# Kernel tuning notes

Measured on AMD Instinct MI355X. Metric: run time of the kernel, lower is better.

The kernel has to match this reference:

```python
import jax, jax.numpy as jnp
import numpy as np

# Model dims (see init_kwargs): embed_dim=64, heads=8, d_k = n_wires = 8
V, D, H, NQ, L, FFN = 32000, 64, 8, 8, 2, 128
B, S = 16, 1024
LAT, H1, H2, NC = 32, 128, 64, 10
INV_SQRT_DK = 1.0 / float(np.sqrt(NQ))
LN_EPS = 1e-5


def _pos_encoding(s, d):
    pos = jnp.arange(s, dtype=jnp.float32)[:, None]
    div = jnp.exp(jnp.arange(0, d, 2, dtype=jnp.float32) * (-np.log(10000.0) / d))
    pe = jnp.zeros((s, d), dtype=jnp.float32)
    pe = pe.at[:, 0::2].set(jnp.sin(pos * div))
    pe = pe.at[:, 1::2].set(jnp.cos(pos * div))
    return pe


def _layernorm(x, g, b):
    mu = jnp.mean(x, axis=-1, keepdims=True)
    var = jnp.mean(jnp.square(x - mu), axis=-1, keepdims=True)
    return (x - mu) * jax.lax.rsqrt(var + LN_EPS) * g + b


def _quantum_heads(x, theta):
    # Analytic simulation of the per-head 8-qubit VQC:
    #   RX(x_i) RX(theta_i) on wire i, CNOT ring (0->1..6->7, 7->0), measure Z.
    # Heisenberg picture: <Z_j> = prod_{i=0..j} cos(x_i+theta_i) for j>=1,
    # <Z_0> = prod_{i=1..7} cos(x_i+theta_i).
    b, s, _ = x.shape
    a = x.reshape(b, s, H, NQ) + theta            # [B,S,H,NQ]
    c = jnp.cos(a)
    cp = jnp.cumprod(c, axis=-1)
    z0 = jnp.prod(c[..., 1:], axis=-1, keepdims=True)
    return jnp.concatenate([z0, cp[..., 1:]], axis=-1)  # [B,S,H,NQ]


def _quantum_attention(x, theta, combine_W):
    qkv = _quantum_heads(x, theta)                 # [B,S,H,dk]
    q = qkv.transpose(0, 2, 1, 3)                  # [B,H,S,dk]
    scores = jnp.einsum('bhqd,bhkd->bhqk', q, q) * INV_SQRT_DK
    p = jax.nn.softmax(scores, axis=-1)
    out = jnp.einsum('bhqk,bhkd->bhqd', p, q)
    out = out.transpose(0, 2, 1, 3).reshape(x.shape[0], x.shape[1], D)
    return out @ combine_W.T                       # no bias (use_bias=False)


def _quantum_ffn(x, theta, W1, b1, W2, b2):
    # FFN QLayer: RX(x_i) then RY(theta_i), no entanglement -> <Z_i> = cos(theta_i)*cos(x_i)
    # GeneralEncoder only reads the first NQ features of each token.
    z = jnp.cos(x[..., :NQ]) * jnp.cos(theta)      # [B,S,NQ]
    h = jax.nn.relu(z @ W1.T + b1)                 # linear1 then ReLU
    return h @ W2.T + b2                           # linear2


def _forward(tokens, emb_table, attn_theta, combine_W, ln1_g, ln1_b, ln2_g, ln2_b,
             ffn_theta, ffn_W1, ffn_b1, ffn_W2, ffn_b2,
             enc_W1, enc_b1, enc_W2, enc_b2, enc_W3, enc_b3,
             dec_W1, dec_b1, dec_W2, dec_b2, dec_W3, dec_b3, cls_W, cls_b):
    x = emb_table[tokens] + _pos_encoding(tokens.shape[1], D)  # embed + positional
    for l in range(L):  # fixed small number of structurally distinct blocks
        a = _quantum_attention(x, attn_theta[l], combine_W[l])
        x = _layernorm(x + a, ln1_g[l], ln1_b[l])
        f = _quantum_ffn(x, ffn_theta[l], ffn_W1[l], ffn_b1[l], ffn_W2[l], ffn_b2[l])
        x = _layernorm(x + f, ln2_g[l], ln2_b[l])
    pooled = jnp.mean(x, axis=1)                   # [B,D]
    # AutoencoderQuantumNet.forward = decode(encode(x)) (quantum_ffn unused there)
    h = jax.nn.relu(pooled @ enc_W1.T + enc_b1)
    h = jax.nn.relu(h @ enc_W2.T + enc_b2)
    lat = h @ enc_W3.T + enc_b3
    h = jax.nn.relu(lat @ dec_W1.T + dec_b1)
    h = jax.nn.relu(h @ dec_W2.T + dec_b2)
    rec = h @ dec_W3.T + dec_b3                    # [B,D]
    return rec @ cls_W.T + cls_b                   # [B,NC]


def setup_inputs() -> dict:
    key = jax.random.key(0)
    ks = list(jax.random.split(key, 32))
    it = iter(ks)
    def nrm(shape, scale=0.05):
        return (jax.random.normal(next(it), shape) * scale).astype(jnp.float32)
    return {
        'tokens': jax.random.randint(next(it), (B, S), 0, V),
        'emb_table': nrm((V, D), 0.02),
        'attn_theta': nrm((L, NQ), 0.1),
        'combine_W': nrm((L, D, D)),
        'ln1_g': jnp.ones((L, D), jnp.float32), 'ln1_b': jnp.zeros((L, D), jnp.float32),
        'ln2_g': jnp.ones((L, D), jnp.float32), 'ln2_b': jnp.zeros((L, D), jnp.float32),
        'ffn_theta': nrm((L, NQ), 0.1),
        'ffn_W1': nrm((L, FFN, NQ)), 'ffn_b1': jnp.zeros((L, FFN), jnp.float32),
        'ffn_W2': nrm((L, D, FFN)), 'ffn_b2': jnp.zeros((L, D), jnp.float32),
        'enc_W1': nrm((H1, D)), 'enc_b1': jnp.zeros((H1,), jnp.float32),
        'enc_W2': nrm((H2, H1)), 'enc_b2': jnp.zeros((H2,), jnp.float32),
        'enc_W3': nrm((LAT, H2)), 'enc_b3': jnp.zeros((LAT,), jnp.float32),
        'dec_W1': nrm((H2, LAT)), 'dec_b1': jnp.zeros((H2,), jnp.float32),
        'dec_W2': nrm((H1, H2)), 'dec_b2': jnp.zeros((H1,), jnp.float32),
        'dec_W3': nrm((D, H1)), 'dec_b3': jnp.zeros((D,), jnp.float32),
        'cls_W': nrm((NC, D)), 'cls_b': jnp.zeros((NC,), jnp.float32),
    }


def reference(tokens, emb_table, attn_theta, combine_W, ln1_g, ln1_b, ln2_g, ln2_b,
              ffn_theta, ffn_W1, ffn_b1, ffn_W2, ffn_b2,
              enc_W1, enc_b1, enc_W2, enc_b2, enc_W3, enc_b3,
              dec_W1, dec_b1, dec_W2, dec_b2, dec_W3, dec_b3, cls_W, cls_b):
    return _forward(tokens, emb_table, attn_theta, combine_W, ln1_g, ln1_b, ln2_g, ln2_b,
                    ffn_theta, ffn_W1, ffn_b1, ffn_W2, ffn_b2,
                    enc_W1, enc_b1, enc_W2, enc_b2, enc_W3, enc_b3,
                    dec_W1, dec_b1, dec_W2, dec_b2, dec_W3, dec_b3, cls_W, cls_b)
```

## Files before the change

kernel.cpp:

```cpp
#include <hip/hip_runtime.h>
#include <math.h>

typedef _Float16 h2 __attribute__((ext_vector_type(2)));
typedef __fp16 hh4 __attribute__((ext_vector_type(4)));
typedef float f4 __attribute__((ext_vector_type(4)));

#define Bsz 16
#define Ssz 1024
#define TOKENS (Bsz * Ssz)
#define Dd 64
#define Hh 8
#define QTTS 520

#if __has_builtin(__builtin_amdgcn_exp2f)
  #define EXPFN(x) __builtin_amdgcn_exp2f(x)
  #define SQRT_PRESCALE 0.7141921f
#else
  #define EXPFN(x) __expf(x)
  #define SQRT_PRESCALE 0.5946036f
#endif

#if __has_builtin(__builtin_amdgcn_mfma_f32_16x16x16_f16)
  #define MFMA16(a, b, c) __builtin_amdgcn_mfma_f32_16x16x16_f16(a, b, c, 0, 0, 0)
#else
  #define MFMA16(a, b, c) __builtin_amdgcn_mfma_f32_16x16x16f16(a, b, c, 0, 0, 0)
#endif

__device__ __forceinline__ h2 pkrtz(float a, float b) {
#if __has_builtin(__builtin_amdgcn_cvt_pkrtz)
  return __builtin_bit_cast(h2, __builtin_amdgcn_cvt_pkrtz(a, b));
#else
  h2 r; r.x = (_Float16)a; r.y = (_Float16)b; return r;
#endif
}
__device__ __forceinline__ unsigned int as_u32(h2 v) {
  return __builtin_bit_cast(unsigned int, v);
}
__device__ __forceinline__ hh4 bc4(uint2 u) {
  return __builtin_bit_cast(hh4, u);
}

__device__ __forceinline__ void qheads_v(const float* xa, const float* th, float* o) {
  float c0 = __cosf(xa[0] + th[0]), c1 = __cosf(xa[1] + th[1]);
  float c2 = __cosf(xa[2] + th[2]), c3 = __cosf(xa[3] + th[3]);
  float c4 = __cosf(xa[4] + th[4]), c5 = __cosf(xa[5] + th[5]);
  float c6 = __cosf(xa[6] + th[6]), c7 = __cosf(xa[7] + th[7]);
  float cp = c0;
  cp *= c1; o[1] = cp; cp *= c2; o[2] = cp; cp *= c3; o[3] = cp;
  cp *= c4; o[4] = cp; cp *= c5; o[5] = cp; cp *= c6; o[6] = cp;
  cp *= c7; o[7] = cp;
  o[0] = c1 * c2 * c3 * c4 * c5 * c6 * c7;
}

template <int EMBED>
__global__ __launch_bounds__(256, 4) void attn_kernel(
    const float* __restrict__ x, float* __restrict__ xw,
    const int* __restrict__ tokens, const float* __restrict__ emb,
    const float* __restrict__ theta,
    float* __restrict__ o_out, float* __restrict__ ps_out) {
  __shared__ unsigned int qrs[Ssz * 4 + 2];
  __shared__ unsigned int qtt[9 * QTTS];
  int blk = blockIdx.x;
  int bh = blk >> 3, split = blk & 7;
  int b = bh >> 3, h = bh & 7;
  int t = threadIdx.x;

  float th[8];
#pragma unroll
  for (int i = 0; i < 8; i++) th[i] = theta[i];

  float frq[4];
  if (EMBED) {
#pragma unroll
    for (int j = 0; j < 4; j++)
      frq[j] = __expf((float)(2 * (h * 4 + j)) * (-0.14391156831f));
  }

  const float* xb = x + (size_t)b * Ssz * Dd + h * 8;

#pragma unroll
  for (int i = 0; i < 4; i += 2) {
    int k0 = t * 4 + i;
    float xa[8], xc[8];
    if (EMBED) {
      int tokA = tokens[b * Ssz + k0];
      int tokB = tokens[b * Ssz + k0 + 1];
      float4 e0 = *(const float4*)&emb[(size_t)tokA * Dd + h * 8];
      float4 e1 = *(const float4*)&emb[(size_t)tokA * Dd + h * 8 + 4];
      float4 f0 = *(const float4*)&emb[(size_t)tokB * Dd + h * 8];
      float4 f1 = *(const float4*)&emb[(size_t)tokB * Dd + h * 8 + 4];
      float sn, cs;
      __sincosf((float)k0 * frq[0], &sn, &cs); xa[0] = e0.x + sn; xa[1] = e0.y + cs;
      __sincosf((float)k0 * frq[1], &sn, &cs); xa[2] = e0.z + sn; xa[3] = e0.w + cs;
      __sincosf((float)k0 * frq[2], &sn, &cs); xa[4] = e1.x + sn; xa[5] = e1.y + cs;
      __sincosf((float)k0 * frq[3], &sn, &cs); xa[6] = e1.z + sn; xa[7] = e1.w + cs;
      __sincosf((float)(k0 + 1) * frq[0], &sn, &cs); xc[0] = f0.x + sn; xc[1] = f0.y + cs;
      __sincosf((float)(k0 + 1) * frq[1], &sn, &cs); xc[2] = f0.z + sn; xc[3] = f0.w + cs;
      __sincosf((float)(k0 + 1) * frq[2], &sn, &cs); xc[4] = f1.x + sn; xc[5] = f1.y + cs;
      __sincosf((float)(k0 + 1) * frq[3], &sn, &cs); xc[6] = f1.z + sn; xc[7] = f1.w + cs;
      if (split == 0) {
        float4 w0, w1;
        w0.x = xa[0]; w0.y = xa[1]; w0.z = xa[2]; w0.w = xa[3];
        w1.x = xa[4]; w1.y = xa[5]; w1.z = xa[6]; w1.w = xa[7];
        *(float4*)&xw[((size_t)b * Ssz + k0) * Dd + h * 8] = w0;
        *(float4*)&xw[((size_t)b * Ssz + k0) * Dd + h * 8 + 4] = w1;
        w0.x = xc[0]; w0.y = xc[1]; w0.z = xc[2]; w0.w = xc[3];
        w1.x = xc[4]; w1.y = xc[5]; w1.z = xc[6]; w1.w = xc[7];
        *(float4*)&xw[((size_t)b * Ssz + k0 + 1) * Dd + h * 8] = w0;
        *(float4*)&xw[((size_t)b * Ssz + k0 + 1) * Dd + h * 8 + 4] = w1;
      }
    } else {
      float4 v0 = *(const float4*)(xb + (size_t)k0 * Dd);
      float4 v1 = *(const float4*)(xb + (size_t)k0 * Dd + 4);
      float4 v2 = *(const float4*)(xb + (size_t)(k0 + 1) * Dd);
      float4 v3 = *(const float4*)(xb + (size_t)(k0 + 1) * Dd + 4);
      xa[0] = v0.x; xa[1] = v0.y; xa[2] = v0.z; xa[3] = v0.w;
      xa[4] = v1.x; xa[5] = v1.y; xa[6] = v1.z; xa[7] = v1.w;
      xc[0] = v2.x; xc[1] = v2.y; xc[2] = v2.z; xc[3] = v2.w;
      xc[4] = v3.x; xc[5] = v3.y; xc[6] = v3.z; xc[7] = v3.w;
    }
    float oa[8], ob[8];
    qheads_v(xa, th, oa);
    qheads_v(xc, th, ob);
    uint4 wa, wb;
    wa.x = as_u32(pkrtz(oa[0] * SQRT_PRESCALE, oa[1] * SQRT_PRESCALE));
    wa.y = as_u32(pkrtz(oa[2] * SQRT_PRESCALE, oa[3] * SQRT_PRESCALE));
    wa.z = as_u32(pkrtz(oa[4] * SQRT_PRESCALE, oa[5] * SQRT_PRESCALE));
    wa.w = as_u32(pkrtz(oa[6] * SQRT_PRESCALE, oa[7] * SQRT_PRESCALE));
    wb.x = as_u32(pkrtz(ob[0] * SQRT_PRESCALE, ob[1] * SQRT_PRESCALE));
    wb.y = as_u32(pkrtz(ob[2] * SQRT_PRESCALE, ob[3] * SQRT_PRESCALE));
    wb.z = as_u32(pkrtz(ob[4] * SQRT_PRESCALE, ob[5] * SQRT_PRESCALE));
    wb.w = as_u32(pkrtz(ob[6] * SQRT_PRESCALE, ob[7] * SQRT_PRESCALE));
    *(uint4*)&qrs[k0 * 4] = wa;
    *(uint4*)&qrs[(k0 + 1) * 4] = wb;
#pragma unroll
    for (int d = 0; d < 8; d++)
      qtt[d * QTTS + (k0 >> 1)] = as_u32(pkrtz(oa[d], ob[d]));
  }
  for (int j = 8 * QTTS + t; j < 9 * QTTS; j += 256) qtt[j] = 0x3C003C00u;
  if (t == 0) { qrs[Ssz * 4] = 0; qrs[Ssz * 4 + 1] = 0; }
  __syncthreads();

  int l = t & 63, w = t >> 6;
  int g = l >> 4, rr = l & 15;
  int rt0 = split * 8 + w * 2;
  int rowA = rt0 * 16 + rr;
  int rowB = rowA + 16;
  uint2 z2; z2.x = 0; z2.y = 0;
  uint2 buA = (g < 2) ? *(const uint2*)&qrs[rowA * 4 + 2 * g] : z2;
  uint2 buB = (g < 2) ? *(const uint2*)&qrs[rowB * 4 + 2 * g] : z2;
  hh4 BrA = bc4(buA), BrB = bc4(buB);
  int aoff  = (g < 2) ? (rr * 4 + 2 * g) : (Ssz * 4);
  int astep = (g < 2) ? 64 : 0;
  int qrow  = (rr >= 8) ? 8 : rr;
  int qoff  = qrow * QTTS + 2 * g;
  f4 zf = {0.f, 0.f, 0.f, 0.f};
  f4 accA0 = zf, accB0 = zf, accA1 = zf, accB1 = zf;

#pragma unroll 4
  for (int kt = 0; kt < 64; kt += 2) {
    uint2 au0 = *(const uint2*)&qrs[aoff + kt * astep];
    uint2 au1 = *(const uint2*)&qrs[aoff + (kt + 1) * astep];
    uint2 qt0 = *(const uint2*)&qtt[qoff + kt * 8];
    uint2 qt1 = *(const uint2*)&qtt[qoff + (kt + 1) * 8];
    {
      hh4 Ak = bc4(au0);
      f4 sA = MFMA16(Ak, BrA, zf);
      f4 sB = MFMA16(Ak, BrB, zf);
      float pA0 = EXPFN(sA.x), pA1 = EXPFN(sA.y), pA2 = EXPFN(sA.z), pA3 = EXPFN(sA.w);
      float pB0 = EXPFN(sB.x), pB1 = EXPFN(sB.y), pB2 = EXPFN(sB.z), pB3 = EXPFN(sB.w);
      uint2 pbA, pbB;
      pbA.x = as_u32(pkrtz(pA0, pA1)); pbA.y = as_u32(pkrtz(pA2, pA3));
      pbB.x = as_u32(pkrtz(pB0, pB1)); pbB.y = as_u32(pkrtz(pB2, pB3));
      hh4 Aq = bc4(qt0);
      accA0 = MFMA16(Aq, bc4(pbA), accA0);
      accB0 = MFMA16(Aq, bc4(pbB), accB0);
    }
    {
      hh4 Ak = bc4(au1);
      f4 sA = MFMA16(Ak, BrA, zf);
      f4 sB = MFMA16(Ak, BrB, zf);
      float pA0 = EXPFN(sA.x), pA1 = EXPFN(sA.y), pA2 = EXPFN(sA.z), pA3 = EXPFN(sA.w);
      float pB0 = EXPFN(sB.x), pB1 = EXPFN(sB.y), pB2 = EXPFN(sB.z), pB3 = EXPFN(sB.w);
      uint2 pbA, pbB;
      pbA.x = as_u32(pkrtz(pA0, pA1)); pbA.y = as_u32(pkrtz(pA2, pA3));
      pbB.x = as_u32(pkrtz(pB0, pB1)); pbB.y = as_u32(pkrtz(pB2, pB3));
      hh4 Aq = bc4(qt1);
      accA1 = MFMA16(Aq, bc4(pbA), accA1);
      accB1 = MFMA16(Aq, bc4(pbB), accB1);
    }
  }
  f4 accA = accA0 + accA1;
  f4 accB = accB0 + accB1;

  size_t tokA = (size_t)b * Ssz + rowA;
  size_t tokB = (size_t)b * Ssz + rowB;
  if (g < 2) {
    *(f4*)&o_out[tokA * 64 + h * 8 + 4 * g] = accA;
    *(f4*)&o_out[tokB * 64 + h * 8 + 4 * g] = accB;
  } else if (g == 2) {
    ps_out[tokA * 8 + h] = accA.x;
    ps_out[tokB * 8 + h] = accB.x;
  }
}

__global__ __launch_bounds__(64) void tail_kernel(
    float* __restrict__ x, const float* __restrict__ o_out,
    const float* __restrict__ ps_out, const float* __restrict__ Wc,
    const float* __restrict__ g1, const float* __restrict__ bb1,
    const float* __restrict__ g2, const float* __restrict__ bb2,
    const float* __restrict__ fth,
    const float* __restrict__ W1, const float* __restrict__ fb1,
    const float* __restrict__ W2, const float* __restrict__ fb2,
    float* __restrict__ partial, int do_partial) {
  __shared__ float xbuf[16][68];
  int l = threadIdx.x & 63;
  int g = l >> 4, c = l & 15;
  int tok0 = blockIdx.x * 16;
  f4 zf = {0.f, 0.f, 0.f, 0.f};

  {
    hh4 Bf[4][4];
#pragma unroll
    for (int dc = 0; dc < 4; dc++)
#pragma unroll
      for (int kc = 0; kc < 4; kc++) {
        float4 wv = *(const float4*)&Wc[(size_t)(dc * 16 + c) * 64 + kc * 16 + 4 * g];
        uint2 u; u.x = as_u32(pkrtz(wv.x, wv.y)); u.y = as_u32(pkrtz(wv.z, wv.w));
        Bf[kc][dc] = bc4(u);
      }
    int tka = tok0 + c;
    hh4 Af[4];
#pragma unroll
    for (int kc = 0; kc < 4; kc++) {
      float4 o4 = *(const float4*)&o_out[(size_t)tka * 64 + kc * 16 + 4 * g];
      float inv = 1.0f / ps_out[(size_t)tka * 8 + kc * 2 + (g >> 1)];
      uint2 u;
      u.x = as_u32(pkrtz(o4.x * inv, o4.y * inv));
      u.y = as_u32(pkrtz(o4.z * inv, o4.w * inv));
      Af[kc] = bc4(u);
    }
    float yy[4][4];
#pragma unroll
    for (int dc = 0; dc < 4; dc++) {
      f4 acc = zf;
#pragma unroll
      for (int kc = 0; kc < 4; kc++) acc = MFMA16(Af[kc], Bf[kc][dc], acc);
      yy[dc][0] = acc.x; yy[dc][1] = acc.y; yy[dc][2] = acc.z; yy[dc][3] = acc.w;
    }
    float g1v[4], b1v[4];
#pragma unroll
    for (int dc = 0; dc < 4; dc++) { g1v[dc] = g1[dc * 16 + c]; b1v[dc] = bb1[dc * 16 + c]; }
#pragma unroll
    for (int r = 0; r < 4; r++) {
      int tok = tok0 + 4 * g + r;
      float rv0 = x[(size_t)tok * 64 + c]      + yy[0][r];
      float rv1 = x[(size_t)tok * 64 + 16 + c] + yy[1][r];
      float rv2 = x[(size_t)tok * 64 + 32 + c] + yy[2][r];
      float rv3 = x[(size_t)tok * 64 + 48 + c] + yy[3][r];
      float s = (rv0 + rv1) + (rv2 + rv3);
      s += __shfl_xor(s, 1, 64); s += __shfl_xor(s, 2, 64);
      s += __shfl_xor(s, 4, 64); s += __shfl_xor(s, 8, 64);
      float mu = s * (1.f / 64.f);
      float t0 = rv0 - mu, t1 = rv1 - mu, t2 = rv2 - mu, t3 = rv3 - mu;
      float q = (t0 * t0 + t1 * t1) + (t2 * t2 + t3 * t3);
      q += __shfl_xor(q, 1, 64); q += __shfl_xor(q, 2, 64);
      q += __shfl_xor(q, 4, 64); q += __shfl_xor(q, 8, 64);
      float inv = rsqrtf(q * (1.f / 64.f) + 1e-5f);
      int tk = 4 * g + r;
      xbuf[tk][c]      = t0 * inv * g1v[0] + b1v[0];
      xbuf[tk][16 + c] = t1 * inv * g1v[1] + b1v[1];
      xbuf[tk][32 + c] = t2 * inv * g1v[2] + b1v[2];
      xbuf[tk][48 + c] = t3 * inv * g1v[3] + b1v[3];
    }
  }

  float4 x4[4];
#pragma unroll
  for (int dc = 0; dc < 4; dc++)
    x4[dc] = *(const float4*)&xbuf[c][dc * 16 + 4 * g];

  uint2 uz; uz.x = 0; uz.y = 0;
  if (g < 2) {
    float4 thv = *(const float4*)&fth[4 * g];
    float z0 = __cosf(x4[0].x) * __cosf(thv.x);
    float z1 = __cosf(x4[0].y) * __cosf(thv.y);
    float z2 = __cosf(x4[0].z) * __cosf(thv.z);
    float z3 = __cosf(x4[0].w) * __cosf(thv.w);
    uz.x = as_u32(pkrtz(z0, z1)); uz.y = as_u32(pkrtz(z2, z3));
  }
  hh4 Bz = bc4(uz);

  hh4 Bh[8];
#pragma unroll
  for (int jc = 0; jc < 8; jc++) {
    uint2 uw; uw.x = 0; uw.y = 0;
    if (g < 2) {
      float4 wv = *(const float4*)&W1[(size_t)(jc * 16 + c) * 8 + 4 * g];
      uw.x = as_u32(pkrtz(wv.x, wv.y)); uw.y = as_u32(pkrtz(wv.z, wv.w));
    }
    f4 d1 = MFMA16(bc4(uw), Bz, zf);
    float4 b1v = *(const float4*)&fb1[jc * 16 + 4 * g];
    float h0 = fmaxf(d1.x + b1v.x, 0.f);
    float h1 = fmaxf(d1.y + b1v.y, 0.f);
    float h2 = fmaxf(d1.z + b1v.z, 0.f);
    float h3 = fmaxf(d1.w + b1v.w, 0.f);
    uint2 uh;
    uh.x = as_u32(pkrtz(h0, h1)); uh.y = as_u32(pkrtz(h2, h3));
    Bh[jc] = bc4(uh);
  }

  float ff[4][4];
#pragma unroll
  for (int dc = 0; dc < 4; dc++) {
    f4 acc = zf;
#pragma unroll
    for (int kc = 0; kc < 8; kc++) {
      float4 wv = *(const float4*)&W2[(size_t)(dc * 16 + c) * 128 + kc * 16 + 4 * g];
      uint2 uw;
      uw.x = as_u32(pkrtz(wv.x, wv.y)); uw.y = as_u32(pkrtz(wv.z, wv.w));
      acc = MFMA16(bc4(uw), Bh[kc], acc);
    }
    ff[dc][0] = acc.x; ff[dc][1] = acc.y; ff[dc][2] = acc.z; ff[dc][3] = acc.w;
  }

  float r2[4][4];
  float s = 0.f;
#pragma unroll
  for (int dc = 0; dc < 4; dc++) {
    float4 b2v = *(const float4*)&fb2[dc * 16 + 4 * g];
    r2[dc][0] = x4[dc].x + ff[dc][0] + b2v.x;
    r2[dc][1] = x4[dc].y + ff[dc][1] + b2v.y;
    r2[dc][2] = x4[dc].z + ff[dc][2] + b2v.z;
    r2[dc][3] = x4[dc].w + ff[dc][3] + b2v.w;
    s += (r2[dc][0] + r2[dc][1]) + (r2[dc][2] + r2[dc][3]);
  }
  s += __shfl_xor(s, 16, 64); s += __shfl_xor(s, 32, 64);
  float mu = s * (1.f / 64.f);
  float q = 0.f;
#pragma unroll
  for (int dc = 0; dc < 4; dc++) {
#pragma unroll
    for (int r = 0; r < 4; r++) { r2[dc][r] -= mu; q += r2[dc][r] * r2[dc][r]; }
  }
  q += __shfl_xor(q, 16, 64); q += __shfl_xor(q, 32, 64);
  float inv = rsqrtf(q * (1.f / 64.f) + 1e-5f);

  float xo[4][4];
#pragma unroll
  for (int dc = 0; dc < 4; dc++) {
    float4 gv = *(const float4*)&g2[dc * 16 + 4 * g];
    float4 bv = *(const float4*)&bb2[dc * 16 + 4 * g];
    xo[dc][0] = r2[dc][0] * inv * gv.x + bv.x;
    xo[dc][1] = r2[dc][1] * inv * gv.y + bv.y;
    xo[dc][2] = r2[dc][2] * inv * gv.z + bv.z;
    xo[dc][3] = r2[dc][3] * inv * gv.w + bv.w;
    float4 o4;
    o4.x = xo[dc][0]; o4.y = xo[dc][1]; o4.z = xo[dc][2]; o4.w = xo[dc][3];
    *(float4*)&x[(size_t)(tok0 + c) * 64 + dc * 16 + 4 * g] = o4;
  }

  if (do_partial) {
#pragma unroll
    for (int dc = 0; dc < 4; dc++)
#pragma unroll
      for (int r = 0; r < 4; r++) {
        float p = xo[dc][r];
        p += __shfl_xor(p, 1, 64); p += __shfl_xor(p, 2, 64);
        p += __shfl_xor(p, 4, 64); p += __shfl_xor(p, 8, 64);
        xo[dc][r] = p;
      }
    if (c == 0) {
#pragma unroll
      for (int dc = 0; dc < 4; dc++) {
        float4 o4;
        o4.x = xo[dc][0]; o4.y = xo[dc][1]; o4.z = xo[dc][2]; o4.w = xo[dc][3];
        *(float4*)&partial[(size_t)blockIdx.x * 64 + dc * 16 + 4 * g] = o4;
      }
    }
  }
}

__global__ __launch_bounds__(128) void head_kernel(
    const float* __restrict__ partial,
    const float* eW1, const float* eb1, const float* eW2, const float* eb2,
    const float* eW3, const float* eb3, const float* dW1, const float* db1v,
    const float* dW2, const float* db2v, const float* dW3, const float* db3v,
    const float* cW, const float* cb, float* __restrict__ out) {
  __shared__ float bufP[64];
  __shared__ float bufA[128];
  __shared__ float bufB[128];
  int b = blockIdx.x, t = threadIdx.x;
  if (t < 64) {
    float s = 0.f;
    for (int c = 0; c < 64; ++c) s += partial[(size_t)(b * 64 + c) * 64 + t];
    bufP[t] = s * (1.f / 1024.f);
  }
  __syncthreads();
  {
    float v = eb1[t];
    for (int d = 0; d < 64; d++) v = fmaf(bufP[d], eW1[t * 64 + d], v);
    bufA[t] = fmaxf(v, 0.f);
  }
  __syncthreads();
  if (t < 64) {
    float v = eb2[t];
    for (int j = 0; j < 128; j++) v = fmaf(bufA[j], eW2[t * 128 + j], v);
    bufB[t] = fmaxf(v, 0.f);
  }
  __syncthreads();
  if (t < 32) {
    float v = eb3[t];
    for (int d = 0; d < 64; d++) v = fmaf(bufB[d], eW3[t * 64 + d], v);
    bufA[t] = v;
  }
  __syncthreads();
  if (t < 64) {
    float v = db1v[t];
    for (int k = 0; k < 32; k++) v = fmaf(bufA[k], dW1[t * 32 + k], v);
    bufB[t] = fmaxf(v, 0.f);
  }
  __syncthreads();
  {
    float v = db2v[t];
    for (int k = 0; k < 64; k++) v = fmaf(bufB[k], dW2[t * 64 + k], v);
    bufA[t] = fmaxf(v, 0.f);
  }
  __syncthreads();
  if (t < 64) {
    float v = db3v[t];
    for (int j = 0; j < 128; j++) v = fmaf(bufA[j], dW3[t * 128 + j], v);
    bufB[t] = v;
  }
  __syncthreads();
  if (t < 10) {
    float v = cb[t];
    for (int d = 0; d < 64; d++) v = fmaf(bufB[d], cW[t * 64 + d], v);
    out[b * 10 + t] = v;
  }
}

extern "C" void kernel_launch(void* const* d_in, const int* in_sizes, int n_in,
                              void* d_out, int out_size, void* d_ws, size_t ws_size,
                              hipStream_t stream) {
  const int*   tokens     = (const int*)d_in[0];
  const float* emb        = (const float*)d_in[1];
  const float* attn_theta = (const float*)d_in[2];
  const float* combine_W  = (const float*)d_in[3];
  const float* ln1_g      = (const float*)d_in[4];
  const float* ln1_b      = (const float*)d_in[5];
  const float* ln2_g      = (const float*)d_in[6];
  const float* ln2_b      = (const float*)d_in[7];
  const float* ffn_theta  = (const float*)d_in[8];
  const float* ffn_W1     = (const float*)d_in[9];
  const float* ffn_b1     = (const float*)d_in[10];
  const float* ffn_W2     = (const float*)d_in[11];
  const float* ffn_b2     = (const float*)d_in[12];
  const float* enc_W1 = (const float*)d_in[13]; const float* enc_b1 = (const float*)d_in[14];
  const float* enc_W2 = (const float*)d_in[15]; const float* enc_b2 = (const float*)d_in[16];
  const float* enc_W3 = (const float*)d_in[17]; const float* enc_b3 = (const float*)d_in[18];
  const float* dec_W1 = (const float*)d_in[19]; const float* dec_b1 = (const float*)d_in[20];
  const float* dec_W2 = (const float*)d_in[21]; const float* dec_b2 = (const float*)d_in[22];
  const float* dec_W3 = (const float*)d_in[23]; const float* dec_b3 = (const float*)d_in[24];
  const float* cls_W  = (const float*)d_in[25]; const float* cls_b  = (const float*)d_in[26];

  float* x       = (float*)d_ws;
  float* o_out   = x + (size_t)TOKENS * 64;
  float* ps_out  = o_out + (size_t)TOKENS * 64;
  float* partial = ps_out + (size_t)TOKENS * 8;
  float* out     = (float*)d_out;

  attn_kernel<1><<<128 * 8, 256, 0, stream>>>(x, x, tokens, emb,
                                              attn_theta, o_out, ps_out);
  tail_kernel<<<TOKENS / 16, 64, 0, stream>>>(
      x, o_out, ps_out, combine_W,
      ln1_g, ln1_b, ln2_g, ln2_b,
      ffn_theta, ffn_W1, ffn_b1, ffn_W2, ffn_b2, partial, 0);
  attn_kernel<0><<<128 * 8, 256, 0, stream>>>(x, x, tokens, emb,
                                              attn_theta + 8, o_out, ps_out);
  tail_kernel<<<TOKENS / 16, 64, 0, stream>>>(
      x, o_out, ps_out, combine_W + 4096,
      ln1_g + 64, ln1_b + 64, ln2_g + 64, ln2_b + 64,
      ffn_theta + 8, ffn_W1 + 1024, ffn_b1 + 128,
      ffn_W2 + 8192, ffn_b2 + 64, partial, 1);
  head_kernel<<<16, 128, 0, stream>>>(partial, enc_W1, enc_b1, enc_W2, enc_b2,
                                      enc_W3, enc_b3, dec_W1, dec_b1, dec_W2,
                                      dec_b2, dec_W3, dec_b3, cls_W, cls_b, out);
}
```

Measured before the change: 87.42 us.

## Process four query row tiles per wave to reuse key/value LDS loads

```diff
diff --git a/kernel.cpp b/kernel.cpp
--- a/kernel.cpp
+++ b/kernel.cpp
@@ -53,7 +53,7 @@
 }
 
 template <int EMBED>
-__global__ __launch_bounds__(256, 4) void attn_kernel(
+__global__ __launch_bounds__(256, 2) void attn_kernel(
     const float* __restrict__ x, float* __restrict__ xw,
     const int* __restrict__ tokens, const float* __restrict__ emb,
     const float* __restrict__ theta,
@@ -61,7 +61,7 @@
   __shared__ unsigned int qrs[Ssz * 4 + 2];
   __shared__ unsigned int qtt[9 * QTTS];
   int blk = blockIdx.x;
-  int bh = blk >> 3, split = blk & 7;
+  int bh = blk >> 2, split = blk & 3;
   int b = bh >> 3, h = bh & 7;
   int t = threadIdx.x;
 
@@ -143,64 +143,56 @@
 
   int l = t & 63, w = t >> 6;
   int g = l >> 4, rr = l & 15;
-  int rt0 = split * 8 + w * 2;
-  int rowA = rt0 * 16 + rr;
-  int rowB = rowA + 16;
+  int rt0 = split * 16 + w * 4;
+  int row0 = rt0 * 16 + rr;
   uint2 z2; z2.x = 0; z2.y = 0;
-  uint2 buA = (g < 2) ? *(const uint2*)&qrs[rowA * 4 + 2 * g] : z2;
-  uint2 buB = (g < 2) ? *(const uint2*)&qrs[rowB * 4 + 2 * g] : z2;
-  hh4 BrA = bc4(buA), BrB = bc4(buB);
+  hh4 Br[4];
+#pragma unroll
+  for (int j = 0; j < 4; j++) {
+    uint2 bu = (g < 2) ? *(const uint2*)&qrs[(row0 + 16 * j) * 4 + 2 * g] : z2;
+    Br[j] = bc4(bu);
+  }
   int aoff  = (g < 2) ? (rr * 4 + 2 * g) : (Ssz * 4);
   int astep = (g < 2) ? 64 : 0;
   int qrow  = (rr >= 8) ? 8 : rr;
   int qoff  = qrow * QTTS + 2 * g;
   f4 zf = {0.f, 0.f, 0.f, 0.f};
-  f4 accA0 = zf, accB0 = zf, accA1 = zf, accB1 = zf;
-
-#pragma unroll 4
-  for (int kt = 0; kt < 64; kt += 2) {
-    uint2 au0 = *(const uint2*)&qrs[aoff + kt * astep];
-    uint2 au1 = *(const uint2*)&qrs[aoff + (kt + 1) * astep];
-    uint2 qt0 = *(const uint2*)&qtt[qoff + kt * 8];
-    uint2 qt1 = *(const uint2*)&qtt[qoff + (kt + 1) * 8];
-    {
-      hh4 Ak = bc4(au0);
-      f4 sA = MFMA16(Ak, BrA, zf);
-      f4 sB = MFMA16(Ak, BrB, zf);
-      float pA0 = EXPFN(sA.x), pA1 = EXPFN(sA.y), pA2 = EXPFN(sA.z), pA3 = EXPFN(sA.w);
-      float pB0 = EXPFN(sB.x), pB1 = EXPFN(sB.y), pB2 = EXPFN(sB.z), pB3 = EXPFN(sB.w);
-      uint2 pbA, pbB;
-      pbA.x = as_u32(pkrtz(pA0, pA1)); pbA.y = as_u32(pkrtz(pA2, pA3));
-      pbB.x = as_u32(pkrtz(pB0, pB1)); pbB.y = as_u32(pkrtz(pB2, pB3));
-      hh4 Aq = bc4(qt0);
-      accA0 = MFMA16(Aq, bc4(pbA), accA0);
-      accB0 = MFMA16(Aq, bc4(pbB), accB0);
-    }
-    {
-      hh4 Ak = bc4(au1);
-      f4 sA = MFMA16(Ak, BrA, zf);
-      f4 sB = MFMA16(Ak, BrB, zf);
-      float pA0 = EXPFN(sA.x), pA1 = EXPFN(sA.y), pA2 = EXPFN(sA.z), pA3 = EXPFN(sA.w);
-      float pB0 = EXPFN(sB.x), pB1 = EXPFN(sB.y), pB2 = EXPFN(sB.z), pB3 = EXPFN(sB.w);
-      uint2 pbA, pbB;
-      pbA.x = as_u32(pkrtz(pA0, pA1)); pbA.y = as_u32(pkrtz(pA2, pA3));
-      pbB.x = as_u32(pkrtz(pB0, pB1)); pbB.y = as_u32(pkrtz(pB2, pB3));
-      hh4 Aq = bc4(qt1);
-      accA1 = MFMA16(Aq, bc4(pbA), accA1);
-      accB1 = MFMA16(Aq, bc4(pbB), accB1);
-    }
-  }
-  f4 accA = accA0 + accA1;
-  f4 accB = accB0 + accB1;
-
-  size_t tokA = (size_t)b * Ssz + rowA;
-  size_t tokB = (size_t)b * Ssz + rowB;
-  if (g < 2) {
-    *(f4*)&o_out[tokA * 64 + h * 8 + 4 * g] = accA;
-    *(f4*)&o_out[tokB * 64 + h * 8 + 4 * g] = accB;
-  } else if (g == 2) {
-    ps_out[tokA * 8 + h] = accA.x;
-    ps_out[tokB * 8 + h] = accB.x;
+  f4 acc0 = zf, acc1 = zf, acc2 = zf, acc3 = zf;
+
+#pragma unroll 2
+  for (int kt = 0; kt < 64; ++kt) {
+    uint2 au = *(const uint2*)&qrs[aoff + kt * astep];
+    uint2 qt = *(const uint2*)&qtt[qoff + kt * 8];
+    hh4 Ak = bc4(au);
+    hh4 Aq = bc4(qt);
+    f4 s0 = MFMA16(Ak, Br[0], zf);
+    f4 s1 = MFMA16(Ak, Br[1], zf);
+    f4 s2 = MFMA16(Ak, Br[2], zf);
+    f4 s3 = MFMA16(Ak, Br[3], zf);
+    uint2 pb0, pb1, pb2, pb3;
+    pb0.x = as_u32(pkrtz(EXPFN(s0.x), EXPFN(s0.y)));
+    pb0.y = as_u32(pkrtz(EXPFN(s0.z), EXPFN(s0.w)));
+    pb1.x = as_u32(pkrtz(EXPFN(s1.x), EXPFN(s1.y)));
+    pb1.y = as_u32(pkrtz(EXPFN(s1.z), EXPFN(s1.w)));
+    pb2.x = as_u32(pkrtz(EXPFN(s2.x), EXPFN(s2.y)));
+    pb2.y = as_u32(pkrtz(EXPFN(s2.z), EXPFN(s2.w)));
+    pb3.x = as_u32(pkrtz(EXPFN(s3.x), EXPFN(s3.y)));
+    pb3.y = as_u32(pkrtz(EXPFN(s3.z), EXPFN(s3.w)));
+    acc0 = MFMA16(Aq, bc4(pb0), acc0);
+    acc1 = MFMA16(Aq, bc4(pb1), acc1);
+    acc2 = MFMA16(Aq, bc4(pb2), acc2);
+    acc3 = MFMA16(Aq, bc4(pb3), acc3);
+  }
+
+#pragma unroll
+  for (int j = 0; j < 4; j++) {
+    f4 acc = (j == 0) ? acc0 : (j == 1) ? acc1 : (j == 2) ? acc2 : acc3;
+    size_t tok = (size_t)b * Ssz + row0 + 16 * j;
+    if (g < 2) {
+      *(f4*)&o_out[tok * 64 + h * 8 + 4 * g] = acc;
+    } else if (g == 2) {
+      ps_out[tok * 8 + h] = acc.x;
+    }
   }
 }
 
@@ -470,13 +462,13 @@
   float* partial = ps_out + (size_t)TOKENS * 8;
   float* out     = (float*)d_out;
 
-  attn_kernel<1><<<128 * 8, 256, 0, stream>>>(x, x, tokens, emb,
+  attn_kernel<1><<<128 * 4, 256, 0, stream>>>(x, x, tokens, emb,
                                               attn_theta, o_out, ps_out);
   tail_kernel<<<TOKENS / 16, 64, 0, stream>>>(
       x, o_out, ps_out, combine_W,
       ln1_g, ln1_b, ln2_g, ln2_b,
       ffn_theta, ffn_W1, ffn_b1, ffn_W2, ffn_b2, partial, 0);
-  attn_kernel<0><<<128 * 8, 256, 0, stream>>>(x, x, tokens, emb,
+  attn_kernel<0><<<128 * 4, 256, 0, stream>>>(x, x, tokens, emb,
                                               attn_theta + 8, o_out, ps_out);
   tail_kernel<<<TOKENS / 16, 64, 0, stream>>>(
       x, o_out, ps_out, combine_W + 4096,
```

Result: slower. 90.90 us (+4.0%).
